# Kernel optimization log

Hardware: AMD Instinct MI355X
Metric: run time of the kernel (lower is better)

The kernel has to match this reference:

```python
import jax, jax.numpy as jnp
import numpy as np

K = 3
PAD = 1
EPS = 1e-5


def _conv2d(x, w, b):
    y = jax.lax.conv_general_dilated(x, w, window_strides=(1, 1), padding='SAME',
                                     dimension_numbers=('NCHW', 'OIHW', 'NCHW'))
    return y + b[None, :, None, None]


def _bn(x, g, beta, m, v):
    inv = jax.lax.rsqrt(v + EPS)
    return (x - m[None, :, None, None]) * (g * inv)[None, :, None, None] + beta[None, :, None, None]


def _deform_conv2d(x, offset, w, b):
    # torchvision deform_conv2d (v1, no mask), stride=1, pad=1, 3x3 kernel.
    B, Cin, H, W = x.shape
    Cout = w.shape[0]
    # offset: [B, 2*K*K, H, W] -> (dy, dx) per kernel tap
    off = offset.reshape(B, K * K, 2, H, W)
    dy, dx = off[:, :, 0], off[:, :, 1]                     # [B, K2, H, W]
    ii, jj = jnp.meshgrid(jnp.arange(K), jnp.arange(K), indexing='ij')
    ki = (ii.reshape(-1) - PAD).astype(x.dtype)             # [K2]
    kj = (jj.reshape(-1) - PAD).astype(x.dtype)
    py = jnp.arange(H, dtype=x.dtype)[None, None, :, None] + ki[None, :, None, None] + dy
    px = jnp.arange(W, dtype=x.dtype)[None, None, None, :] + kj[None, :, None, None] + dx
    y0 = jnp.floor(py)
    x0 = jnp.floor(px)
    wy = py - y0
    wx = px - x0
    flat = x.reshape(B, Cin, H * W)

    def gather(yc, xc):
        valid = ((yc >= 0) & (yc < H) & (xc >= 0) & (xc < W)).astype(x.dtype)
        yi = jnp.clip(yc, 0, H - 1).astype(jnp.int32)
        xi = jnp.clip(xc, 0, W - 1).astype(jnp.int32)
        idx = (yi * W + xi).reshape(B, -1)                  # [B, K2*H*W]
        g = jax.vmap(lambda f, i: f[:, i])(flat, idx)       # [B, Cin, K2*H*W]
        return g.reshape(B, Cin, K * K, H, W) * valid[:, None]

    v = (gather(y0,     x0    ) * ((1 - wy) * (1 - wx))[:, None]
         + gather(y0,     x0 + 1) * ((1 - wy) * wx)[:, None]
         + gather(y0 + 1, x0    ) * (wy * (1 - wx))[:, None]
         + gather(y0 + 1, x0 + 1) * (wy * wx)[:, None])     # [B, Cin, K2, H, W]
    out = jnp.einsum('bckhw,ock->bohw', v, w.reshape(Cout, Cin, K * K))
    return out + b[None, :, None, None]


def setup_inputs() -> dict:
    key = jax.random.key(0)
    ks = jax.random.split(key, 12)
    d = {}
    d['x'] = jax.random.normal(ks[0], (32, 3, 64, 64), jnp.float32)
    d['offset1_w'] = jax.random.normal(ks[1], (18, 3, 3, 3), jnp.float32) * 0.05
    d['offset1_b'] = jnp.zeros((18,), jnp.float32)
    d['conv1_w'] = jax.random.normal(ks[2], (64, 3, 3, 3), jnp.float32) * 0.1
    d['conv1_b'] = jnp.zeros((64,), jnp.float32)
    d['bn1_gamma'] = jnp.ones((64,), jnp.float32)
    d['bn1_beta'] = jnp.zeros((64,), jnp.float32)
    d['bn1_mean'] = jnp.zeros((64,), jnp.float32)
    d['bn1_var'] = jax.random.uniform(ks[3], (64,), jnp.float32, 0.5, 1.5)
    d['offset2_w'] = jax.random.normal(ks[4], (18, 64, 3, 3), jnp.float32) * 0.02
    d['offset2_b'] = jnp.zeros((18,), jnp.float32)
    d['conv2_w'] = jax.random.normal(ks[5], (128, 64, 3, 3), jnp.float32) * 0.05
    d['conv2_b'] = jnp.zeros((128,), jnp.float32)
    d['bn2_gamma'] = jnp.ones((128,), jnp.float32)
    d['bn2_beta'] = jnp.zeros((128,), jnp.float32)
    d['bn2_mean'] = jnp.zeros((128,), jnp.float32)
    d['bn2_var'] = jax.random.uniform(ks[6], (128,), jnp.float32, 0.5, 1.5)
    d['fc1_w'] = jax.random.normal(ks[7], (256, 128), jnp.float32) * 0.08
    d['fc1_b'] = jnp.zeros((256,), jnp.float32)
    d['fc2_w'] = jax.random.normal(ks[8], (200, 256), jnp.float32) * 0.06
    d['fc2_b'] = jnp.zeros((200,), jnp.float32)
    return d


def reference(x, offset1_w, offset1_b, conv1_w, conv1_b, bn1_gamma, bn1_beta, bn1_mean, bn1_var,
              offset2_w, offset2_b, conv2_w, conv2_b, bn2_gamma, bn2_beta, bn2_mean, bn2_var,
              fc1_w, fc1_b, fc2_w, fc2_b):
    # Eval-mode forward (dropout layers are identity / deterministic).
    off1 = _conv2d(x, offset1_w, offset1_b)
    h = _deform_conv2d(x, off1, conv1_w, conv1_b)
    h = jax.nn.relu(_bn(h, bn1_gamma, bn1_beta, bn1_mean, bn1_var))
    off2 = _conv2d(h, offset2_w, offset2_b)
    h = _deform_conv2d(h, off2, conv2_w, conv2_b)
    h = jax.nn.relu(_bn(h, bn2_gamma, bn2_beta, bn2_mean, bn2_var))
    h = h.mean(axis=(2, 3))                                 # global avg pool -> [B, 128]
    h = jax.nn.relu(h @ fc1_w.T + fc1_b)
    return h @ fc2_w.T + fc2_b
```

## Files before the change

### kernel.cpp

```cpp
#include <hip/hip_runtime.h>

#define EPS 1e-5f

#define W1OT 0
#define W1B  1024
#define W2T  4096
#define W2OB 40960
#define SC1  59392
#define SH1  59456
#define SC2  59520
#define SH2  59648
#define POOL 59776
#define XP   65536
#define H1B  589824
#define W1B_U   2048
#define W2T_U   8192
#define W2OB_U  81920
#define H1B_U   1179648

typedef __attribute__((ext_vector_type(8))) short bhalf8;
typedef __attribute__((ext_vector_type(8))) unsigned short u16x8;
typedef __attribute__((ext_vector_type(4))) float f32x4;

#define BPAD 72
#define OPAD2 296
#define APAD 40

struct Tap { int i00, i01, i10, i11; float w00, w01, w10, w11; };

__device__ __forceinline__ Tap make_tap(float py, float px) {
    float y0f = floorf(py), x0f = floorf(px);
    float wy = py - y0f, wx = px - x0f;
    bool by0 = (y0f >= 0.f)  && (y0f < 64.f);
    bool by1 = (y0f >= -1.f) && (y0f < 63.f);
    bool bx0 = (x0f >= 0.f)  && (x0f < 64.f);
    bool bx1 = (x0f >= -1.f) && (x0f < 63.f);
    int y0 = min(max((int)y0f, 0), 63);
    int y1 = min(max((int)y0f + 1, 0), 63);
    int x0 = min(max((int)x0f, 0), 63);
    int x1 = min(max((int)x0f + 1, 0), 63);
    Tap tp;
    tp.i00 = y0 * 64 + x0; tp.i01 = y0 * 64 + x1;
    tp.i10 = y1 * 64 + x0; tp.i11 = y1 * 64 + x1;
    tp.w00 = (by0 && bx0) ? (1.f - wy) * (1.f - wx) : 0.f;
    tp.w01 = (by0 && bx1) ? (1.f - wy) * wx         : 0.f;
    tp.w10 = (by1 && bx0) ? wy * (1.f - wx)         : 0.f;
    tp.w11 = (by1 && bx1) ? wy * wx                 : 0.f;
    return tp;
}

__device__ __forceinline__ ushort f2bf(float f) {
    union { float f; uint u; } a; a.f = f;
    uint u = a.u;
    return (ushort)((u + 0x7fffu + ((u >> 16) & 1u)) >> 16);
}
__device__ __forceinline__ float bf2f(ushort u) {
    union { uint u; float f; } a; a.u = ((uint)u) << 16;
    return a.f;
}

__global__ __launch_bounds__(256) void k_prep(
    const float* __restrict__ x,
    const float* __restrict__ o1w, const float* __restrict__ c1w,
    const float* __restrict__ o2w, const float* __restrict__ c2w,
    const float* __restrict__ c1b, const float* __restrict__ g1,
    const float* __restrict__ be1, const float* __restrict__ m1,
    const float* __restrict__ v1,
    const float* __restrict__ c2b, const float* __restrict__ g2,
    const float* __restrict__ be2, const float* __restrict__ m2,
    const float* __restrict__ v2,
    float* __restrict__ ws) {
    int tid = blockIdx.x * 256 + threadIdx.x;
    ushort* wsu = (ushort*)ws;
    if (tid < 648) {
        int co = tid % 18, tc = tid / 18, c = tc & 3, t = tc >> 2;
        ws[W1OT + tid] = (c < 3) ? o1w[(co * 3 + c) * 9 + t] : 0.f;
    } else if (tid < 2696) {
        int i = tid - 648;
        int n = i >> 5, k = i & 31;
        float v = 0.f;
        if (k < 27) { int c = k % 3, t = k / 3; v = c1w[(n * 3 + c) * 9 + t]; }
        wsu[W1B_U + i] = f2bf(v);
    } else if (tid < 76424) {
        int i = tid - 2696;
        int c = i & 63, n = (i >> 6) & 127, t = i >> 13;
        wsu[W2T_U + i] = f2bf(c2w[(n * 64 + c) * 9 + t]);
    } else if (tid < 94856) {
        int i = tid - 76424;
        int n = i / 576, k = i - n * 576;
        int c = k & 63, t = k >> 6;
        float v = (n < 18) ? o2w[(n * 64 + c) * 9 + t] : 0.f;
        wsu[W2OB_U + i] = f2bf(v);
    } else if (tid < 94920) {
        int i = tid - 94856;
        float s = g1[i] * rsqrtf(v1[i] + EPS);
        ws[SC1 + i] = s;
        ws[SH1 + i] = (c1b[i] - m1[i]) * s + be1[i];
    } else if (tid < 95048) {
        int i = tid - 94920;
        float s = g2[i] * rsqrtf(v2[i] + EPS);
        ws[SC2 + i] = s;
        ws[SH2 + i] = (c2b[i] - m2[i]) * s + be2[i];
    } else if (tid < 99144) {
        ws[POOL + tid - 95048] = 0.f;
    } else if (tid < 230216) {
        int i = tid - 99144;
        int b = i >> 12, hw = i & 4095;
        const float* xpp = x + (size_t)b * 3 * 4096 + hw;
        f32x4 o;
        o[0] = xpp[0]; o[1] = xpp[4096]; o[2] = xpp[8192]; o[3] = 0.f;
        *(f32x4*)(ws + XP + (size_t)i * 4) = o;
    }
}

__global__ __launch_bounds__(256, 4) void k_def1(
    const float* __restrict__ o1b, float* __restrict__ ws) {
    __shared__ ushort Alds[256 * APAD];
    __shared__ ushort Blds[64 * APAD];
    __shared__ float wo[648];
    __shared__ float scl[128];
    int tid = threadIdx.x;
    for (int i = tid; i < 648; i += 256) wo[i] = ws[W1OT + i];
    if (tid < 128) scl[tid] = ws[SC1 + tid];
    {
        const ushort* src = (const ushort*)ws + W1B_U;
        if (tid < 128) {
            int n = tid >> 1, half = (tid & 1) * 16;
            *(uint4*)(Blds + n * APAD + half)     = *(const uint4*)(src + n * 32 + half);
            *(uint4*)(Blds + n * APAD + half + 8) = *(const uint4*)(src + n * 32 + half + 8);
        }
    }
    int g = blockIdx.x;
    int b = (g & 7) * 4 + ((g >> 3) & 3);
    int row0 = (g >> 5) * 4;
    int h = row0 + (tid >> 6), w = tid & 63;
    const float* xp = ws + XP + (size_t)b * 16384;

    float off[18];
#pragma unroll
    for (int i = 0; i < 18; ++i) off[i] = o1b[i];
    __syncthreads();
#pragma unroll
    for (int t = 0; t < 9; ++t) {
        int yy = h + t / 3 - 1, xx = w + t % 3 - 1;
        f32x4 pv = (f32x4)0.f;
        if (yy >= 0 && yy < 64 && xx >= 0 && xx < 64)
            pv = *(const f32x4*)(xp + (yy * 64 + xx) * 4);
#pragma unroll
        for (int c = 0; c < 3; ++c) {
            const float* wp = wo + (t * 4 + c) * 18;
#pragma unroll
            for (int co = 0; co < 18; ++co) off[co] += pv[c] * wp[co];
        }
    }
    ushort ob[32];
#pragma unroll
    for (int i = 0; i < 32; ++i) ob[i] = 0;
#pragma unroll
    for (int t = 0; t < 9; ++t) {
        Tap tp = make_tap((float)(h + t / 3 - 1) + off[2 * t],
                          (float)(w + t % 3 - 1) + off[2 * t + 1]);
        f32x4 c00 = *(const f32x4*)(xp + tp.i00 * 4);
        f32x4 c01 = *(const f32x4*)(xp + tp.i01 * 4);
        f32x4 c10 = *(const f32x4*)(xp + tp.i10 * 4);
        f32x4 c11 = *(const f32x4*)(xp + tp.i11 * 4);
        f32x4 vt = tp.w00 * c00 + tp.w01 * c01 + tp.w10 * c10 + tp.w11 * c11;
        ob[t * 3 + 0] = f2bf(vt[0]);
        ob[t * 3 + 1] = f2bf(vt[1]);
        ob[t * 3 + 2] = f2bf(vt[2]);
    }
    {
        ushort* ar = Alds + tid * APAD;
#pragma unroll
        for (int i = 0; i < 4; ++i)
            *(uint4*)(ar + i * 8) = *(const uint4*)(ob + i * 8);
    }
    __syncthreads();

    int lane = tid & 63, wv = tid >> 6;
    int r = lane & 15, q = lane >> 4;
    bhalf8 bf[4];
#pragma unroll
    for (int nt = 0; nt < 4; ++nt)
        bf[nt] = *(const bhalf8*)(Blds + (nt * 16 + r) * APAD + q * 8);
    f32x4 acc[4][4];
#pragma unroll
    for (int mt = 0; mt < 4; ++mt) {
        bhalf8 af = *(const bhalf8*)(Alds + (wv * 64 + mt * 16 + r) * APAD + q * 8);
#pragma unroll
        for (int nt = 0; nt < 4; ++nt)
            acc[mt][nt] = __builtin_amdgcn_mfma_f32_16x16x32_bf16(af, bf[nt], (f32x4)0.f, 0, 0, 0);
    }
    ushort* hb = (ushort*)ws + H1B_U + (size_t)(b * 4096 + row0 * 64) * 64;
#pragma unroll
    for (int nt = 0; nt < 4; ++nt) {
        int col = nt * 16 + r;
        float s0 = scl[col], s1 = scl[64 + col];
#pragma unroll
        for (int mt = 0; mt < 4; ++mt) {
            int pxl = wv * 64 + mt * 16 + q * 4;
#pragma unroll
            for (int rr = 0; rr < 4; ++rr)
                hb[(size_t)(pxl + rr) * 64 + col] =
                    f2bf(fmaxf(acc[mt][nt][rr] * s0 + s1, 0.f));
        }
    }
}

__global__ __launch_bounds__(256, 4) void k_def2(
    const float* __restrict__ o2b, float* __restrict__ ws) {
    __shared__ ushort smem[11520];
    ushort* Bo   = smem;
    float* offL  = (float*)smem;
    ushort* Bdef = smem + 2304;
    int g = blockIdx.x;
    int b = (g & 7) * 4 + ((g >> 3) & 3);
    int row = g >> 5;
    int tid = threadIdx.x, lane = tid & 63, wv = tid >> 6;
    int r = lane & 15, q = lane >> 4;
    int px = wv * 16 + r;
    const ushort* hb = (const ushort*)ws + H1B_U + (size_t)b * 262144;
    const ushort* wB = (const ushort*)ws + W2T_U;
    const ushort* bt = (const ushort*)ws + W2OB_U;

    f32x4 acc2[2];
    acc2[0] = (f32x4)0.f; acc2[1] = (f32x4)0.f;
#pragma unroll
    for (int kh = 0; kh < 2; ++kh) {
        if (kh) __syncthreads();
        for (int i = tid; i < 1152; i += 256) {
            int n = i / 36, j = i - n * 36;
            int jc = j * 8, t = jc >> 5, cc = jc & 31;
            *(uint4*)(Bo + n * OPAD2 + jc) =
                *(const uint4*)(bt + n * 576 + t * 64 + kh * 32 + cc);
        }
        __syncthreads();
#pragma unroll
        for (int t = 0; t < 9; ++t) {
            int yy = row + t / 3 - 1;
            int xx = px + t % 3 - 1;
            bool val = (yy >= 0 && yy < 64 && xx >= 0 && xx < 64);
            int yyc = min(max(yy, 0), 63), xxc = min(max(xx, 0), 63);
            const ushort* ap = hb + (size_t)(yyc * 64 + xxc) * 64 + kh * 32 + q * 8;
            bhalf8 af = val ? *(const bhalf8*)(ap) : (bhalf8)(short)0;
#pragma unroll
            for (int nt = 0; nt < 2; ++nt) {
                bhalf8 bf = *(const bhalf8*)(Bo + (nt * 16 + r) * OPAD2 + t * 32 + q * 8);
                acc2[nt] = __builtin_amdgcn_mfma_f32_16x16x32_bf16(af, bf, acc2[nt], 0, 0, 0);
            }
        }
    }
    __syncthreads();
#pragma unroll
    for (int nt = 0; nt < 2; ++nt) {
        int n = nt * 16 + r;
        if (n < 18) {
            float bias = o2b[n];
#pragma unroll
            for (int rr = 0; rr < 4; ++rr)
                offL[(wv * 16 + q * 4 + rr) * 18 + n] = acc2[nt][rr] + bias;
        }
    }
    __syncthreads();

    f32x4 acc[8];
#pragma unroll
    for (int j = 0; j < 8; ++j) acc[j] = (f32x4)0.f;
    int bn = tid >> 1, bc = (tid & 1) * 32;

    for (int t = 0; t < 9; ++t) {
        float oy = offL[px * 18 + 2 * t];
        float ox = offL[px * 18 + 2 * t + 1];
        Tap tp = make_tap((float)(row + t / 3 - 1) + oy,
                          (float)(px + t % 3 - 1) + ox);
        if (t) __syncthreads();
        {
            const uint4* s4 = (const uint4*)(wB + (t * 128 + bn) * 64 + bc);
            uint4 p0 = s4[0], p1 = s4[1], p2 = s4[2], p3 = s4[3];
            ushort* dst = Bdef + bn * BPAD + bc;
            *(uint4*)(dst)      = p0;
            *(uint4*)(dst + 8)  = p1;
            *(uint4*)(dst + 16) = p2;
            *(uint4*)(dst + 24) = p3;
        }
        __syncthreads();
#pragma unroll
        for (int ks = 0; ks < 2; ++ks) {
            int ko = ks * 32 + q * 8;
            bhalf8 bf[8];
#pragma unroll
            for (int nt = 0; nt < 8; ++nt)
                bf[nt] = *(const bhalf8*)(Bdef + (nt * 16 + r) * BPAD + ko);
            u16x8 g00 = *(const u16x8*)(hb + (size_t)tp.i00 * 64 + ko);
            u16x8 g01 = *(const u16x8*)(hb + (size_t)tp.i01 * 64 + ko);
            u16x8 g10 = *(const u16x8*)(hb + (size_t)tp.i10 * 64 + ko);
            u16x8 g11 = *(const u16x8*)(hb + (size_t)tp.i11 * 64 + ko);
            f32x4 lo = (f32x4)0.f, hi = (f32x4)0.f;
#pragma unroll
            for (int j = 0; j < 4; ++j) {
                lo[j] = tp.w00 * bf2f(g00[j]) + tp.w01 * bf2f(g01[j])
                      + tp.w10 * bf2f(g10[j]) + tp.w11 * bf2f(g11[j]);
                hi[j] = tp.w00 * bf2f(g00[j + 4]) + tp.w01 * bf2f(g01[j + 4])
                      + tp.w10 * bf2f(g10[j + 4]) + tp.w11 * bf2f(g11[j + 4]);
            }
            bhalf8 af;
#pragma unroll
            for (int j = 0; j < 4; ++j) {
                af[j]     = (short)f2bf(lo[j]);
                af[j + 4] = (short)f2bf(hi[j]);
            }
#pragma unroll
            for (int nt = 0; nt < 8; ++nt)
                acc[nt] = __builtin_amdgcn_mfma_f32_16x16x32_bf16(af, bf[nt], acc[nt], 0, 0, 0);
        }
    }
    const float* sc = ws + SC2;
    const float* sh = ws + SH2;
    float* pool = ws + POOL;
#pragma unroll
    for (int nt = 0; nt < 8; ++nt) {
        int col = nt * 16 + r;
        float s0 = sc[col], s1 = sh[col];
        float s = 0.f;
#pragma unroll
        for (int rr = 0; rr < 4; ++rr)
            s += fmaxf(acc[nt][rr] * s0 + s1, 0.f);
        s += __shfl_xor(s, 16);
        s += __shfl_xor(s, 32);
        if (lane < 16) atomicAdd(&pool[b * 128 + col], s);
    }
}

__global__ __launch_bounds__(256) void k_fc(
    const float* __restrict__ w1, const float* __restrict__ b1,
    const float* __restrict__ w2, const float* __restrict__ b2,
    const float* __restrict__ ws, float* __restrict__ out) {
    int b = blockIdx.x, o = threadIdx.x;
    __shared__ float pl[128];
    __shared__ float hl[256];
    if (o < 128) pl[o] = ws[POOL + b * 128 + o] * (1.f / 4096.f);
    __syncthreads();
    float s = b1[o];
    const float* wp = w1 + o * 128;
#pragma unroll 8
    for (int c = 0; c < 128; ++c) s += pl[c] * wp[c];
    hl[o] = fmaxf(s, 0.f);
    __syncthreads();
    if (o < 200) {
        float s2 = b2[o];
        const float* wp2 = w2 + o * 256;
#pragma unroll 8
        for (int c = 0; c < 256; ++c) s2 += hl[c] * wp2[c];
        out[b * 200 + o] = s2;
    }
}

extern "C" void kernel_launch(void* const* d_in, const int* in_sizes, int n_in,
                              void* d_out, int out_size, void* d_ws, size_t ws_size,
                              hipStream_t stream) {
    const float* x   = (const float*)d_in[0];
    const float* o1w = (const float*)d_in[1];
    const float* o1b = (const float*)d_in[2];
    const float* c1w = (const float*)d_in[3];
    const float* c1b = (const float*)d_in[4];
    const float* g1  = (const float*)d_in[5];
    const float* be1 = (const float*)d_in[6];
    const float* m1  = (const float*)d_in[7];
    const float* v1  = (const float*)d_in[8];
    const float* o2w = (const float*)d_in[9];
    const float* o2b = (const float*)d_in[10];
    const float* c2w = (const float*)d_in[11];
    const float* c2b = (const float*)d_in[12];
    const float* g2  = (const float*)d_in[13];
    const float* be2 = (const float*)d_in[14];
    const float* m2  = (const float*)d_in[15];
    const float* v2  = (const float*)d_in[16];
    const float* f1w = (const float*)d_in[17];
    const float* f1b = (const float*)d_in[18];
    const float* f2w = (const float*)d_in[19];
    const float* f2b = (const float*)d_in[20];
    float* ws  = (float*)d_ws;
    float* out = (float*)d_out;

    k_prep<<<900, 256, 0, stream>>>(x, o1w, c1w, o2w, c2w,
                                    c1b, g1, be1, m1, v1,
                                    c2b, g2, be2, m2, v2, ws);
    k_def1<<<512, 256, 0, stream>>>(o1b, ws);
    k_def2<<<2048, 256, 0, stream>>>(o2b, ws);
    k_fc<<<32, 256, 0, stream>>>(f1w, f1b, f2w, f2b, ws, out);
}
```

Before: 291.9 us.

## Prefetch next-tap bilinear gathers and read conv2 weights directly from global

In the second deformable conv kernel, per-tap offsets are hoisted into registers and the four bilinear-corner gathers for the next tap are software-prefetched while the current tap's MFMAs run. The per-tap staging of the weight tile through shared memory, along with its two barriers per tap, is removed; the weight fragments are now loaded straight from global memory (likely cache-resident) inside the MFMA loop. Shared memory shrinks and the launch-bounds occupancy hint drops from 4 to 2 to leave room for the extra prefetch registers. The trade-off is higher register pressure, fewer resident blocks, and redundant global reads of the weights across waves.

```diff
diff --git a/kernel.cpp b/kernel.cpp
--- a/kernel.cpp
+++ b/kernel.cpp
@@ -22,7 +22,6 @@
 typedef __attribute__((ext_vector_type(8))) unsigned short u16x8;
 typedef __attribute__((ext_vector_type(4))) float f32x4;
 
-#define BPAD 72
 #define OPAD2 296
 #define APAD 40
 
@@ -207,12 +206,11 @@
     }
 }
 
-__global__ __launch_bounds__(256, 4) void k_def2(
+__global__ __launch_bounds__(256, 2) void k_def2(
     const float* __restrict__ o2b, float* __restrict__ ws) {
-    __shared__ ushort smem[11520];
-    ushort* Bo   = smem;
-    float* offL  = (float*)smem;
-    ushort* Bdef = smem + 2304;
+    __shared__ ushort smem[9472];
+    ushort* Bo  = smem;
+    float* offL = (float*)smem;
     int g = blockIdx.x;
     int b = (g & 7) * 4 + ((g >> 3) & 3);
     int row = g >> 5;
@@ -263,45 +261,54 @@
     }
     __syncthreads();
 
+    float2 off[9];
+#pragma unroll
+    for (int t = 0; t < 9; ++t)
+        off[t] = *(const float2*)(offL + px * 18 + 2 * t);
+
     f32x4 acc[8];
 #pragma unroll
     for (int j = 0; j < 8; ++j) acc[j] = (f32x4)0.f;
-    int bn = tid >> 1, bc = (tid & 1) * 32;
-
+
+    Tap tp = make_tap((float)(row - 1) + off[0].x, (float)(px - 1) + off[0].y);
+    u16x8 gl[2][4];
+    {
+        const ushort* p00 = hb + (size_t)tp.i00 * 64 + q * 8;
+        const ushort* p01 = hb + (size_t)tp.i01 * 64 + q * 8;
+        const ushort* p10 = hb + (size_t)tp.i10 * 64 + q * 8;
+        const ushort* p11 = hb + (size_t)tp.i11 * 64 + q * 8;
+        gl[0][0] = *(const u16x8*)(p00);      gl[1][0] = *(const u16x8*)(p00 + 32);
+        gl[0][1] = *(const u16x8*)(p01);      gl[1][1] = *(const u16x8*)(p01 + 32);
+        gl[0][2] = *(const u16x8*)(p10);      gl[1][2] = *(const u16x8*)(p10 + 32);
+        gl[0][3] = *(const u16x8*)(p11);      gl[1][3] = *(const u16x8*)(p11 + 32);
+    }
+
+#pragma unroll
     for (int t = 0; t < 9; ++t) {
-        float oy = offL[px * 18 + 2 * t];
-        float ox = offL[px * 18 + 2 * t + 1];
-        Tap tp = make_tap((float)(row + t / 3 - 1) + oy,
-                          (float)(px + t % 3 - 1) + ox);
-        if (t) __syncthreads();
-        {
-            const uint4* s4 = (const uint4*)(wB + (t * 128 + bn) * 64 + bc);
-            uint4 p0 = s4[0], p1 = s4[1], p2 = s4[2], p3 = s4[3];
-            ushort* dst = Bdef + bn * BPAD + bc;
-            *(uint4*)(dst)      = p0;
-            *(uint4*)(dst + 8)  = p1;
-            *(uint4*)(dst + 16) = p2;
-            *(uint4*)(dst + 24) = p3;
-        }
-        __syncthreads();
+        Tap tpn;
+        u16x8 gn[2][4];
+        if (t < 8) {
+            tpn = make_tap((float)(row + (t + 1) / 3 - 1) + off[t + 1].x,
+                           (float)(px + (t + 1) % 3 - 1) + off[t + 1].y);
+            const ushort* p00 = hb + (size_t)tpn.i00 * 64 + q * 8;
+            const ushort* p01 = hb + (size_t)tpn.i01 * 64 + q * 8;
+            const ushort* p10 = hb + (size_t)tpn.i10 * 64 + q * 8;
+            const ushort* p11 = hb + (size_t)tpn.i11 * 64 + q * 8;
+            gn[0][0] = *(const u16x8*)(p00);  gn[1][0] = *(const u16x8*)(p00 + 32);
+            gn[0][1] = *(const u16x8*)(p01);  gn[1][1] = *(const u16x8*)(p01 + 32);
+            gn[0][2] = *(const u16x8*)(p10);  gn[1][2] = *(const u16x8*)(p10 + 32);
+            gn[0][3] = *(const u16x8*)(p11);  gn[1][3] = *(const u16x8*)(p11 + 32);
+        }
 #pragma unroll
         for (int ks = 0; ks < 2; ++ks) {
             int ko = ks * 32 + q * 8;
-            bhalf8 bf[8];
-#pragma unroll
-            for (int nt = 0; nt < 8; ++nt)
-                bf[nt] = *(const bhalf8*)(Bdef + (nt * 16 + r) * BPAD + ko);
-            u16x8 g00 = *(const u16x8*)(hb + (size_t)tp.i00 * 64 + ko);
-            u16x8 g01 = *(const u16x8*)(hb + (size_t)tp.i01 * 64 + ko);
-            u16x8 g10 = *(const u16x8*)(hb + (size_t)tp.i10 * 64 + ko);
-            u16x8 g11 = *(const u16x8*)(hb + (size_t)tp.i11 * 64 + ko);
             f32x4 lo = (f32x4)0.f, hi = (f32x4)0.f;
 #pragma unroll
             for (int j = 0; j < 4; ++j) {
-                lo[j] = tp.w00 * bf2f(g00[j]) + tp.w01 * bf2f(g01[j])
-                      + tp.w10 * bf2f(g10[j]) + tp.w11 * bf2f(g11[j]);
-                hi[j] = tp.w00 * bf2f(g00[j + 4]) + tp.w01 * bf2f(g01[j + 4])
-                      + tp.w10 * bf2f(g10[j + 4]) + tp.w11 * bf2f(g11[j + 4]);
+                lo[j] = tp.w00 * bf2f(gl[ks][0][j]) + tp.w01 * bf2f(gl[ks][1][j])
+                      + tp.w10 * bf2f(gl[ks][2][j]) + tp.w11 * bf2f(gl[ks][3][j]);
+                hi[j] = tp.w00 * bf2f(gl[ks][0][j + 4]) + tp.w01 * bf2f(gl[ks][1][j + 4])
+                      + tp.w10 * bf2f(gl[ks][2][j + 4]) + tp.w11 * bf2f(gl[ks][3][j + 4]);
             }
             bhalf8 af;
 #pragma unroll
@@ -310,8 +317,17 @@
                 af[j + 4] = (short)f2bf(hi[j]);
             }
 #pragma unroll
-            for (int nt = 0; nt < 8; ++nt)
-                acc[nt] = __builtin_amdgcn_mfma_f32_16x16x32_bf16(af, bf[nt], acc[nt], 0, 0, 0);
+            for (int nt = 0; nt < 8; ++nt) {
+                bhalf8 bf = *(const bhalf8*)(wB + (size_t)(t * 128 + nt * 16 + r) * 64 + ko);
+                acc[nt] = __builtin_amdgcn_mfma_f32_16x16x32_bf16(af, bf, acc[nt], 0, 0, 0);
+            }
+        }
+        if (t < 8) {
+            tp = tpn;
+#pragma unroll
+            for (int ks = 0; ks < 2; ++ks)
+#pragma unroll
+                for (int p = 0; p < 4; ++p) gl[ks][p] = gn[ks][p];
         }
     }
     const float* sc = ws + SC2;
```

New measurement: 393.7 us. 34.9% more time.

## Process two output rows per block in k_def2 to reuse staged weights

Applied to the files above, without the earlier changes.

Each k_def2 block now computes two image rows instead of one, halving the grid to 1024 blocks. The per-tap weight tiles staged in shared memory (offset-conv and deform-conv weights) are reused across both rows, which halves weight staging traffic and the number of barriers per output row. In exchange each thread holds twice the accumulators, and launch bounds drop from 4 to 2 blocks per CU, so occupancy and latency hiding for the bilinear gathers may fall.

```diff
diff --git a/kernel.cpp b/kernel.cpp
--- a/kernel.cpp
+++ b/kernel.cpp
@@ -207,15 +207,15 @@
     }
 }
 
-__global__ __launch_bounds__(256, 4) void k_def2(
+__global__ __launch_bounds__(256, 2) void k_def2(
     const float* __restrict__ o2b, float* __restrict__ ws) {
-    __shared__ ushort smem[11520];
+    __shared__ ushort smem[13824];
     ushort* Bo   = smem;
     float* offL  = (float*)smem;
-    ushort* Bdef = smem + 2304;
+    ushort* Bdef = smem + 4608;
     int g = blockIdx.x;
     int b = (g & 7) * 4 + ((g >> 3) & 3);
-    int row = g >> 5;
+    int row0 = (g >> 5) * 2;
     int tid = threadIdx.x, lane = tid & 63, wv = tid >> 6;
     int r = lane & 15, q = lane >> 4;
     int px = wv * 16 + r;
@@ -223,8 +223,9 @@
     const ushort* wB = (const ushort*)ws + W2T_U;
     const ushort* bt = (const ushort*)ws + W2OB_U;
 
-    f32x4 acc2[2];
-    acc2[0] = (f32x4)0.f; acc2[1] = (f32x4)0.f;
+    f32x4 acc2[2][2];
+#pragma unroll
+    for (int mi = 0; mi < 2; ++mi) { acc2[mi][0] = (f32x4)0.f; acc2[mi][1] = (f32x4)0.f; }
 #pragma unroll
     for (int kh = 0; kh < 2; ++kh) {
         if (kh) __syncthreads();
@@ -237,42 +238,51 @@
         __syncthreads();
 #pragma unroll
         for (int t = 0; t < 9; ++t) {
-            int yy = row + t / 3 - 1;
             int xx = px + t % 3 - 1;
-            bool val = (yy >= 0 && yy < 64 && xx >= 0 && xx < 64);
-            int yyc = min(max(yy, 0), 63), xxc = min(max(xx, 0), 63);
-            const ushort* ap = hb + (size_t)(yyc * 64 + xxc) * 64 + kh * 32 + q * 8;
-            bhalf8 af = val ? *(const bhalf8*)(ap) : (bhalf8)(short)0;
-#pragma unroll
-            for (int nt = 0; nt < 2; ++nt) {
-                bhalf8 bf = *(const bhalf8*)(Bo + (nt * 16 + r) * OPAD2 + t * 32 + q * 8);
-                acc2[nt] = __builtin_amdgcn_mfma_f32_16x16x32_bf16(af, bf, acc2[nt], 0, 0, 0);
+            int xxc = min(max(xx, 0), 63);
+            bhalf8 bf0 = *(const bhalf8*)(Bo + r * OPAD2 + t * 32 + q * 8);
+            bhalf8 bf1 = *(const bhalf8*)(Bo + (16 + r) * OPAD2 + t * 32 + q * 8);
+#pragma unroll
+            for (int mi = 0; mi < 2; ++mi) {
+                int yy = row0 + mi + t / 3 - 1;
+                bool val = (yy >= 0 && yy < 64 && xx >= 0 && xx < 64);
+                int yyc = min(max(yy, 0), 63);
+                const ushort* ap = hb + (size_t)(yyc * 64 + xxc) * 64 + kh * 32 + q * 8;
+                bhalf8 af = val ? *(const bhalf8*)(ap) : (bhalf8)(short)0;
+                acc2[mi][0] = __builtin_amdgcn_mfma_f32_16x16x32_bf16(af, bf0, acc2[mi][0], 0, 0, 0);
+                acc2[mi][1] = __builtin_amdgcn_mfma_f32_16x16x32_bf16(af, bf1, acc2[mi][1], 0, 0, 0);
             }
         }
     }
     __syncthreads();
 #pragma unroll
-    for (int nt = 0; nt < 2; ++nt) {
-        int n = nt * 16 + r;
-        if (n < 18) {
-            float bias = o2b[n];
-#pragma unroll
-            for (int rr = 0; rr < 4; ++rr)
-                offL[(wv * 16 + q * 4 + rr) * 18 + n] = acc2[nt][rr] + bias;
-        }
-    }
-    __syncthreads();
-
-    f32x4 acc[8];
-#pragma unroll
-    for (int j = 0; j < 8; ++j) acc[j] = (f32x4)0.f;
+    for (int mi = 0; mi < 2; ++mi)
+#pragma unroll
+        for (int nt = 0; nt < 2; ++nt) {
+            int n = nt * 16 + r;
+            if (n < 18) {
+                float bias = o2b[n];
+#pragma unroll
+                for (int rr = 0; rr < 4; ++rr)
+                    offL[(mi * 64 + wv * 16 + q * 4 + rr) * 18 + n] = acc2[mi][nt][rr] + bias;
+            }
+        }
+    __syncthreads();
+
+    f32x4 acc[2][8];
+#pragma unroll
+    for (int mi = 0; mi < 2; ++mi)
+#pragma unroll
+        for (int j = 0; j < 8; ++j) acc[mi][j] = (f32x4)0.f;
     int bn = tid >> 1, bc = (tid & 1) * 32;
 
     for (int t = 0; t < 9; ++t) {
-        float oy = offL[px * 18 + 2 * t];
-        float ox = offL[px * 18 + 2 * t + 1];
-        Tap tp = make_tap((float)(row + t / 3 - 1) + oy,
-                          (float)(px + t % 3 - 1) + ox);
+        float2 oA = *(const float2*)(offL + (size_t)px * 18 + 2 * t);
+        float2 oB = *(const float2*)(offL + (size_t)(64 + px) * 18 + 2 * t);
+        Tap tpA = make_tap((float)(row0 + t / 3 - 1) + oA.x,
+                           (float)(px + t % 3 - 1) + oA.y);
+        Tap tpB = make_tap((float)(row0 + 1 + t / 3 - 1) + oB.x,
+                           (float)(px + t % 3 - 1) + oB.y);
         if (t) __syncthreads();
         {
             const uint4* s4 = (const uint4*)(wB + (t * 128 + bn) * 64 + bc);
@@ -291,27 +301,31 @@
 #pragma unroll
             for (int nt = 0; nt < 8; ++nt)
                 bf[nt] = *(const bhalf8*)(Bdef + (nt * 16 + r) * BPAD + ko);
-            u16x8 g00 = *(const u16x8*)(hb + (size_t)tp.i00 * 64 + ko);
-            u16x8 g01 = *(const u16x8*)(hb + (size_t)tp.i01 * 64 + ko);
-            u16x8 g10 = *(const u16x8*)(hb + (size_t)tp.i10 * 64 + ko);
-            u16x8 g11 = *(const u16x8*)(hb + (size_t)tp.i11 * 64 + ko);
-            f32x4 lo = (f32x4)0.f, hi = (f32x4)0.f;
-#pragma unroll
-            for (int j = 0; j < 4; ++j) {
-                lo[j] = tp.w00 * bf2f(g00[j]) + tp.w01 * bf2f(g01[j])
-                      + tp.w10 * bf2f(g10[j]) + tp.w11 * bf2f(g11[j]);
-                hi[j] = tp.w00 * bf2f(g00[j + 4]) + tp.w01 * bf2f(g01[j + 4])
-                      + tp.w10 * bf2f(g10[j + 4]) + tp.w11 * bf2f(g11[j + 4]);
+#pragma unroll
+            for (int mi = 0; mi < 2; ++mi) {
+                const Tap tp = mi ? tpB : tpA;
+                u16x8 g00 = *(const u16x8*)(hb + (size_t)tp.i00 * 64 + ko);
+                u16x8 g01 = *(const u16x8*)(hb + (size_t)tp.i01 * 64 + ko);
+                u16x8 g10 = *(const u16x8*)(hb + (size_t)tp.i10 * 64 + ko);
+                u16x8 g11 = *(const u16x8*)(hb + (size_t)tp.i11 * 64 + ko);
+                f32x4 lo = (f32x4)0.f, hi = (f32x4)0.f;
+#pragma unroll
+                for (int j = 0; j < 4; ++j) {
+                    lo[j] = tp.w00 * bf2f(g00[j]) + tp.w01 * bf2f(g01[j])
+                          + tp.w10 * bf2f(g10[j]) + tp.w11 * bf2f(g11[j]);
+                    hi[j] = tp.w00 * bf2f(g00[j + 4]) + tp.w01 * bf2f(g01[j + 4])
+                          + tp.w10 * bf2f(g10[j + 4]) + tp.w11 * bf2f(g11[j + 4]);
+                }
+                bhalf8 af;
+#pragma unroll
+                for (int j = 0; j < 4; ++j) {
+                    af[j]     = (short)f2bf(lo[j]);
+                    af[j + 4] = (short)f2bf(hi[j]);
+                }
+#pragma unroll
+                for (int nt = 0; nt < 8; ++nt)
+                    acc[mi][nt] = __builtin_amdgcn_mfma_f32_16x16x32_bf16(af, bf[nt], acc[mi][nt], 0, 0, 0);
             }
-            bhalf8 af;
-#pragma unroll
-            for (int j = 0; j < 4; ++j) {
-                af[j]     = (short)f2bf(lo[j]);
-                af[j + 4] = (short)f2bf(hi[j]);
-            }
-#pragma unroll
-            for (int nt = 0; nt < 8; ++nt)
-                acc[nt] = __builtin_amdgcn_mfma_f32_16x16x32_bf16(af, bf[nt], acc[nt], 0, 0, 0);
         }
     }
     const float* sc = ws + SC2;
@@ -323,8 +337,10 @@
         float s0 = sc[col], s1 = sh[col];
         float s = 0.f;
 #pragma unroll
-        for (int rr = 0; rr < 4; ++rr)
-            s += fmaxf(acc[nt][rr] * s0 + s1, 0.f);
+        for (int mi = 0; mi < 2; ++mi)
+#pragma unroll
+            for (int rr = 0; rr < 4; ++rr)
+                s += fmaxf(acc[mi][nt][rr] * s0 + s1, 0.f);
         s += __shfl_xor(s, 16);
         s += __shfl_xor(s, 32);
         if (lane < 16) atomicAdd(&pool[b * 128 + col], s);
@@ -386,6 +402,6 @@
                                     c1b, g1, be1, m1, v1,
                                     c2b, g2, be2, m2, v2, ws);
     k_def1<<<512, 256, 0, stream>>>(o1b, ws);
-    k_def2<<<2048, 256, 0, stream>>>(o2b, ws);
+    k_def2<<<1024, 256, 0, stream>>>(o2b, ws);
     k_fc<<<32, 256, 0, stream>>>(f1w, f1b, f2w, f2b, ws, out);
 }
```

New measurement: 306.7 us. +5.1%, slower.
